# Optimization experiments

Hardware: AMD Instinct MI355X
Metric: run time of the kernel (lower is better)

## Reference

```python
import jax, jax.numpy as jnp
import numpy as np

N_NODES = 100000
N_FEAT = 256
N_HIDDEN = 64
N_EDGES = 3200000
LEAKY_SLOPE = 0.05


def setup_inputs() -> dict:
    key = jax.random.key(0)
    k1, k2, k3, k4, k5 = jax.random.split(key, 5)
    x = jax.random.normal(k1, (N_NODES, N_FEAT), dtype=jnp.float32)
    edge_index = jax.random.randint(k2, (2, N_EDGES), 0, N_NODES, dtype=jnp.int64)
    # params (torch Linear default-like scale)
    W_fc = jax.random.normal(k3, (N_FEAT, N_HIDDEN), dtype=jnp.float32) / np.sqrt(N_FEAT)
    a_w = jax.random.normal(k4, (2 * N_HIDDEN, 1), dtype=jnp.float32) / np.sqrt(2 * N_HIDDEN)
    a_b = jax.random.normal(k5, (1,), dtype=jnp.float32) * 0.01
    return {"x": x, "edge_index": edge_index, "W_fc": W_fc, "a_w": a_w, "a_b": a_b}


def reference(x, edge_index, W_fc, a_w, a_b):
    n = x.shape[0]
    h = x @ W_fc                                  # [N, H]
    src = edge_index[0]
    dst = edge_index[1]
    # a([h_src, h_dst]) == h_src @ a_w[:H] + h_dst @ a_w[H:] + a_b (same math, avoids concat)
    s = h @ a_w[:N_HIDDEN, 0]                     # [N]
    t = h @ a_w[N_HIDDEN:, 0]                     # [N]
    e = s[src] + t[dst] + a_b[0]                  # [E]
    e = jnp.where(e >= 0, e, LEAKY_SLOPE * e)     # LeakyReLU(0.05)
    attention = jnp.exp(e)                        # [E]
    row_sum = jax.ops.segment_sum(attention, src, num_segments=n)  # [N]
    alpha = attention / row_sum[src]              # [E]
    # sparse mm: out[i] = sum_{e: src_e=i} alpha_e * h[dst_e]
    out = jax.ops.segment_sum(alpha[:, None] * h[dst], src, num_segments=n)  # [N, H]
    return out, alpha
```

## Files before the change

kernel.cpp:

```cpp
#include <hip/hip_runtime.h>
#include <hip/hip_fp16.h>
#include <cstdint>
#include <cstddef>

#define NFEAT 256
#define NHID 64
#define SLOPE 0.05f
#define BKTSZ 64
#define NBKT_MAX 1568
#define P1 512
#define DSTBITS 17
#define WTPAD 264
#define SORTBUF 6272
#define BKTCAP 2560

typedef _Float16 half8 __attribute__((ext_vector_type(8)));
typedef float f32x4 __attribute__((ext_vector_type(4)));

__global__ __launch_bounds__(256) void fc_kernel(
    const float* __restrict__ x, const float* __restrict__ W,
    const float* __restrict__ aw,
    __half* __restrict__ h, float* __restrict__ srinv, float* __restrict__ t,
    int nNodes)
{
    __shared__ _Float16 Wt[NHID][WTPAD];

    const int tid = threadIdx.x;

    #pragma unroll 4
    for (int it = 0; it < 16; ++it) {
        const int idx = it * 256 + tid;
        const int n  = idx & 63;
        const int k0 = (idx >> 6) << 2;
        union { _Float16 v[4]; uint2 u; } pk;
        pk.v[0] = (_Float16)W[(k0 + 0) * NHID + n];
        pk.v[1] = (_Float16)W[(k0 + 1) * NHID + n];
        pk.v[2] = (_Float16)W[(k0 + 2) * NHID + n];
        pk.v[3] = (_Float16)W[(k0 + 3) * NHID + n];
        *(uint2*)&Wt[n][k0] = pk.u;
    }
    __syncthreads();

    const int l   = tid & 63;
    const int wv  = tid >> 6;
    const int l16 = l & 15;
    const int q   = l >> 4;
    const int kb8 = q * 8;

    const int blockRow = blockIdx.x * 128;
    const int nClamp = nNodes - 1;
    const int r0c = min(blockRow + wv * 32 + l16,      nClamp);
    const int r1c = min(blockRow + wv * 32 + l16 + 16, nClamp);
    const float* xr0 = x + (size_t)r0c * NFEAT;
    const float* xr1 = x + (size_t)r1c * NFEAT;

    f32x4 acc[2][4];
    #pragma unroll
    for (int m = 0; m < 2; ++m)
        #pragma unroll
        for (int nb = 0; nb < 4; ++nb)
            acc[m][nb] = (f32x4){0.f, 0.f, 0.f, 0.f};

    #pragma unroll
    for (int ks = 0; ks < 8; ++ks) {
        const int k0 = ks * 32 + kb8;
        const float4 fa0 = *(const float4*)(xr0 + k0);
        const float4 fa1 = *(const float4*)(xr0 + k0 + 4);
        const float4 fb0 = *(const float4*)(xr1 + k0);
        const float4 fb1 = *(const float4*)(xr1 + k0 + 4);
        half8 a0, a1;
        a0[0] = (_Float16)fa0.x; a0[1] = (_Float16)fa0.y;
        a0[2] = (_Float16)fa0.z; a0[3] = (_Float16)fa0.w;
        a0[4] = (_Float16)fa1.x; a0[5] = (_Float16)fa1.y;
        a0[6] = (_Float16)fa1.z; a0[7] = (_Float16)fa1.w;
        a1[0] = (_Float16)fb0.x; a1[1] = (_Float16)fb0.y;
        a1[2] = (_Float16)fb0.z; a1[3] = (_Float16)fb0.w;
        a1[4] = (_Float16)fb1.x; a1[5] = (_Float16)fb1.y;
        a1[6] = (_Float16)fb1.z; a1[7] = (_Float16)fb1.w;
        const half8 b0 = *(const half8*)&Wt[ 0 + l16][k0];
        const half8 b1 = *(const half8*)&Wt[16 + l16][k0];
        const half8 b2 = *(const half8*)&Wt[32 + l16][k0];
        const half8 b3 = *(const half8*)&Wt[48 + l16][k0];
        acc[0][0] = __builtin_amdgcn_mfma_f32_16x16x32_f16(a0, b0, acc[0][0], 0, 0, 0);
        acc[0][1] = __builtin_amdgcn_mfma_f32_16x16x32_f16(a0, b1, acc[0][1], 0, 0, 0);
        acc[0][2] = __builtin_amdgcn_mfma_f32_16x16x32_f16(a0, b2, acc[0][2], 0, 0, 0);
        acc[0][3] = __builtin_amdgcn_mfma_f32_16x16x32_f16(a0, b3, acc[0][3], 0, 0, 0);
        acc[1][0] = __builtin_amdgcn_mfma_f32_16x16x32_f16(a1, b0, acc[1][0], 0, 0, 0);
        acc[1][1] = __builtin_amdgcn_mfma_f32_16x16x32_f16(a1, b1, acc[1][1], 0, 0, 0);
        acc[1][2] = __builtin_amdgcn_mfma_f32_16x16x32_f16(a1, b2, acc[1][2], 0, 0, 0);
        acc[1][3] = __builtin_amdgcn_mfma_f32_16x16x32_f16(a1, b3, acc[1][3], 0, 0, 0);
    }

    const float aws0 = aw[l16],      aws1 = aw[16 + l16];
    const float aws2 = aw[32 + l16], aws3 = aw[48 + l16];
    const float awt0 = aw[64 + l16], awt1 = aw[80 + l16];
    const float awt2 = aw[96 + l16], awt3 = aw[112 + l16];

    #pragma unroll
    for (int m = 0; m < 2; ++m) {
        const int rb = blockRow + wv * 32 + m * 16 + q * 4;
        #pragma unroll
        for (int r = 0; r < 4; ++r) {
            const int row = rb + r;
            const bool ok = row < nNodes;
            const float c0 = acc[m][0][r];
            const float c1 = acc[m][1][r];
            const float c2 = acc[m][2][r];
            const float c3 = acc[m][3][r];
            if (ok) {
                __half* hp = &h[(size_t)row * NHID + l16];
                hp[0]  = __float2half(c0);
                hp[16] = __float2half(c1);
                hp[32] = __float2half(c2);
                hp[48] = __float2half(c3);
            }
            float ps = c0 * aws0 + c1 * aws1 + c2 * aws2 + c3 * aws3;
            float pt = c0 * awt0 + c1 * awt1 + c2 * awt2 + c3 * awt3;
            ps += __shfl_xor(ps, 1, 16); pt += __shfl_xor(pt, 1, 16);
            ps += __shfl_xor(ps, 2, 16); pt += __shfl_xor(pt, 2, 16);
            ps += __shfl_xor(ps, 4, 16); pt += __shfl_xor(pt, 4, 16);
            ps += __shfl_xor(ps, 8, 16); pt += __shfl_xor(pt, 8, 16);
            if (ok && l16 == 0) { srinv[2 * row] = ps; t[row] = pt; }
        }
    }
}

__global__ __launch_bounds__(256) void cnt_kernel(
    const int* __restrict__ ei, int E, int CPB, int nbkt, int* __restrict__ cntT)
{
    __shared__ int hist[NBKT_MAX];
    const int g = blockIdx.x;
    const int tid = threadIdx.x;
    for (int i = tid; i < nbkt; i += 256) hist[i] = 0;
    __syncthreads();
    const int beg = g * CPB;
    const int end = min(E, beg + CPB);
    const int c4 = (end - beg) >> 2;
    for (int i = tid; i < c4; i += 256) {
        const int4 v = *(const int4*)&ei[beg + i * 4];
        atomicAdd(&hist[v.x >> 6], 1);
        atomicAdd(&hist[v.y >> 6], 1);
        atomicAdd(&hist[v.z >> 6], 1);
        atomicAdd(&hist[v.w >> 6], 1);
    }
    for (int e = beg + c4 * 4 + tid; e < end; e += 256)
        atomicAdd(&hist[ei[e] >> 6], 1);
    __syncthreads();
    for (int b = tid; b < nbkt; b += 256)
        cntT[b * P1 + g] = hist[b];
}

__global__ __launch_bounds__(256) void scanA_kernel(
    const int* __restrict__ v, int* __restrict__ bsum, int n)
{
    __shared__ int sh[256];
    const int i = blockIdx.x * 256 + threadIdx.x;
    sh[threadIdx.x] = (i < n) ? v[i] : 0;
    __syncthreads();
    #pragma unroll
    for (int off = 128; off > 0; off >>= 1) {
        if (threadIdx.x < off) sh[threadIdx.x] += sh[threadIdx.x + off];
        __syncthreads();
    }
    if (threadIdx.x == 0) bsum[blockIdx.x] = sh[0];
}

__global__ __launch_bounds__(256) void scanC_kernel(
    const int* __restrict__ v, const int* __restrict__ bsum,
    int* __restrict__ outp, int n, int NB)
{
    __shared__ int red[256];
    __shared__ int sh[256];
    __shared__ int base0s;
    const int tid = threadIdx.x;

    int partial = 0;
    for (int j = tid; j < (int)blockIdx.x; j += 256) partial += bsum[j];
    red[tid] = partial;
    __syncthreads();
    #pragma unroll
    for (int off = 128; off > 0; off >>= 1) {
        if (tid < off) red[tid] += red[tid + off];
        __syncthreads();
    }
    if (tid == 0) base0s = red[0];
    __syncthreads();
    const int base0 = base0s;

    const int i = blockIdx.x * 256 + tid;
    const int val = (i < n) ? v[i] : 0;
    sh[tid] = val;
    __syncthreads();
    #pragma unroll
    for (int off = 1; off < 256; off <<= 1) {
        int add = (tid >= off) ? sh[tid - off] : 0;
        __syncthreads();
        sh[tid] += add;
        __syncthreads();
    }
    const int incl = sh[tid];
    if (i < n) outp[i] = base0 + incl - val;
    if (i == n - 1) outp[n] = base0 + incl;
}

__global__ __launch_bounds__(256) void place_kernel(
    const int* __restrict__ ei, int E, int CPB, int nbkt,
    const int* __restrict__ cntT, const int* __restrict__ base,
    int* __restrict__ pairs)
{
    __shared__ int loff[NBKT_MAX + 1];
    __shared__ int cur[NBKT_MAX];
    __shared__ int gb[NBKT_MAX];
    __shared__ int psum[256];
    __shared__ int sorted[SORTBUF];

    const int g = blockIdx.x;
    const int tid = threadIdx.x;
    const int beg = g * CPB;
    const int end = min(E, beg + CPB);
    const int total = end - beg;
    const int CHK = (nbkt + 255) / 256;

    for (int b = tid; b < nbkt; b += 256) {
        loff[b] = cntT[b * P1 + g];
        gb[b]   = base[b * P1 + g];
    }
    __syncthreads();

    {
        int mysum = 0;
        const int b0 = tid * CHK;
        const int b1 = min(b0 + CHK, nbkt);
        for (int b = b0; b < b1; ++b) mysum += loff[b];
        psum[tid] = mysum;
        __syncthreads();
        #pragma unroll
        for (int o = 1; o < 256; o <<= 1) {
            int v = 0;
            if (tid >= o) v = psum[tid - o];
            __syncthreads();
            psum[tid] += v;
            __syncthreads();
        }
        int run = (tid > 0) ? psum[tid - 1] : 0;
        for (int b = b0; b < b1; ++b) {
            const int c = loff[b];
            loff[b] = run;
            cur[b] = run;
            run += c;
        }
        if (tid == 255) loff[nbkt] = run;
    }
    __syncthreads();

    const int c4 = total >> 2;
    for (int i = tid; i < c4; i += 256) {
        const int e = beg + i * 4;
        const int4 s4 = *(const int4*)&ei[e];
        const int4 d4 = *(const int4*)&ei[E + e];
        int p;
        p = atomicAdd(&cur[s4.x >> 6], 1); sorted[p] = ((s4.x & (BKTSZ-1)) << DSTBITS) | d4.x;
        p = atomicAdd(&cur[s4.y >> 6], 1); sorted[p] = ((s4.y & (BKTSZ-1)) << DSTBITS) | d4.y;
        p = atomicAdd(&cur[s4.z >> 6], 1); sorted[p] = ((s4.z & (BKTSZ-1)) << DSTBITS) | d4.z;
        p = atomicAdd(&cur[s4.w >> 6], 1); sorted[p] = ((s4.w & (BKTSZ-1)) << DSTBITS) | d4.w;
    }
    for (int e = beg + c4 * 4 + tid; e < end; e += 256) {
        const int sn = ei[e];
        const int d  = ei[E + e];
        const int p  = atomicAdd(&cur[sn >> 6], 1);
        sorted[p] = ((sn & (BKTSZ-1)) << DSTBITS) | d;
    }
    __syncthreads();

    for (int i = tid; i < total; i += 256) {
        int lo = 0, hi = nbkt;
        #pragma unroll
        for (int it = 0; it < 11; ++it) {
            const int mid = (lo + hi) >> 1;
            if (loff[mid] <= i) lo = mid; else hi = mid;
        }
        pairs[gb[lo] + (i - loff[lo])] = sorted[i];
    }
}

__global__ __launch_bounds__(256) void bagg_kernel(
    const int* __restrict__ pairs, const int* __restrict__ base,
    float* __restrict__ srinv, const float* __restrict__ t,
    const __half* __restrict__ h, const float* __restrict__ ab_p,
    float* __restrict__ out, int nNodes, int nbkt, int E)
{
    __shared__ int cnt[BKTSZ];
    __shared__ int off[BKTSZ];
    __shared__ int cur[BKTSZ];
    __shared__ int sorted[BKTCAP];

    const int bkt = blockIdx.x;
    const int tid = threadIdx.x;
    const int beg = base[bkt * P1];
    const int end = (bkt + 1 < nbkt) ? base[(bkt + 1) * P1] : E;

    if (tid < BKTSZ) cnt[tid] = 0;
    __syncthreads();

    int pr[10];
    int myc = 0;
    #pragma unroll
    for (int k = 0; k < 10; ++k) {
        const int e = beg + k * 256 + tid;
        if (e < end) {
            const int p = pairs[e];
            pr[k] = p;
            atomicAdd(&cnt[p >> DSTBITS], 1);
            myc = k + 1;
        }
    }
    __syncthreads();

    if (tid < BKTSZ) off[tid] = cnt[tid];
    __syncthreads();
    #pragma unroll
    for (int o = 1; o < BKTSZ; o <<= 1) {
        int v = 0;
        if (tid < BKTSZ && tid >= o) v = off[tid - o];
        __syncthreads();
        if (tid < BKTSZ) off[tid] += v;
        __syncthreads();
    }
    if (tid < BKTSZ) cur[tid] = off[tid] - cnt[tid];
    __syncthreads();

    #pragma unroll
    for (int k = 0; k < 10; ++k) {
        if (k < myc) {
            const int p = pr[k];
            const int pos = atomicAdd(&cur[p >> DSTBITS], 1);
            sorted[pos] = p & ((1 << DSTBITS) - 1);
        }
    }
    __syncthreads();

    const int lane = tid & 63;
    const int wv = tid >> 6;
    const int quarter = lane >> 4;
    const int col = lane & 15;
    const float ab = ab_p[0];
    const uint2* hh4 = (const uint2*)h;

    for (int li = wv; li < BKTSZ; li += 4) {
        const int n = (bkt << 6) + li;
        if (n >= nNodes) continue;
        const int endL = off[li];
        const int begL = endL - cnt[li];
        const float sn = srinv[2 * n];
        float part = 0.f;
        float4 acc = {0.f, 0.f, 0.f, 0.f};
        for (int i0 = begL; i0 < endL; i0 += 64) {
            const int my = min(endL - i0, 64);
            int dl = 0; float el = 0.f;
            if (lane < my) {
                dl = sorted[i0 + lane];
                float ev = sn + t[dl] + ab;
                ev = (ev >= 0.f) ? ev : SLOPE * ev;
                el = __expf(ev);
            }
            part += el;
            const int my4 = (my + 3) & ~3;
            int j = 0;
            for (; j + 8 <= my4; j += 8) {
                const int   d0 = __shfl(dl, j + quarter);
                const float e0 = __shfl(el, j + quarter);
                const int   d1 = __shfl(dl, j + 4 + quarter);
                const float e1 = __shfl(el, j + 4 + quarter);
                const uint2 r0 = hh4[(size_t)d0 * 16 + col];
                const uint2 r1 = hh4[(size_t)d1 * 16 + col];
                const float2 lo0 = __half22float2(*(const __half2*)&r0.x);
                const float2 hi0 = __half22float2(*(const __half2*)&r0.y);
                const float2 lo1 = __half22float2(*(const __half2*)&r1.x);
                const float2 hi1 = __half22float2(*(const __half2*)&r1.y);
                acc.x += e0 * lo0.x; acc.y += e0 * lo0.y;
                acc.z += e0 * hi0.x; acc.w += e0 * hi0.y;
                acc.x += e1 * lo1.x; acc.y += e1 * lo1.y;
                acc.z += e1 * hi1.x; acc.w += e1 * hi1.y;
            }
            for (; j < my4; j += 4) {
                const int   d0 = __shfl(dl, j + quarter);
                const float e0 = __shfl(el, j + quarter);
                const uint2 r0 = hh4[(size_t)d0 * 16 + col];
                const float2 lo0 = __half22float2(*(const __half2*)&r0.x);
                const float2 hi0 = __half22float2(*(const __half2*)&r0.y);
                acc.x += e0 * lo0.x; acc.y += e0 * lo0.y;
                acc.z += e0 * hi0.x; acc.w += e0 * hi0.y;
            }
        }
        #pragma unroll
        for (int o = 32; o > 0; o >>= 1) part += __shfl_xor(part, o, 64);
        const float inv = (endL > begL) ? 1.0f / part : 0.f;
        if (lane == 0) srinv[2 * n + 1] = inv;
        acc.x += __shfl_xor(acc.x, 16, 64); acc.x += __shfl_xor(acc.x, 32, 64);
        acc.y += __shfl_xor(acc.y, 16, 64); acc.y += __shfl_xor(acc.y, 32, 64);
        acc.z += __shfl_xor(acc.z, 16, 64); acc.z += __shfl_xor(acc.z, 32, 64);
        acc.w += __shfl_xor(acc.w, 16, 64); acc.w += __shfl_xor(acc.w, 32, 64);
        if (quarter == 0) {
            float4 o4;
            o4.x = acc.x * inv; o4.y = acc.y * inv;
            o4.z = acc.z * inv; o4.w = acc.w * inv;
            *(float4*)&out[(size_t)n * NHID + col * 4] = o4;
        }
    }
}

__global__ __launch_bounds__(256) void alpha_kernel(
    const int* __restrict__ ei, const float* __restrict__ srinv,
    const float* __restrict__ t,
    const float* __restrict__ ab_p, float* __restrict__ alpha, int E)
{
    const float ab = ab_p[0];
    const int gid = blockIdx.x * blockDim.x + threadIdx.x;
    const int step = gridDim.x * blockDim.x;
    const int E4 = E >> 2;

    #define AEDGE(sn, d) ({                                                 \
        const float2 sr = *(const float2*)&srinv[2 * (sn)];                 \
        float ev = sr.x + t[d] + ab;                                        \
        ev = (ev >= 0.f) ? ev : SLOPE * ev;                                 \
        __expf(ev) * sr.y; })

    for (int i = gid; i < E4; i += step) {
        const int e = i * 4;
        const int4 s4 = *(const int4*)&ei[e];
        const int4 d4 = *(const int4*)&ei[E + e];
        float4 a;
        a.x = AEDGE(s4.x, d4.x);
        a.y = AEDGE(s4.y, d4.y);
        a.z = AEDGE(s4.z, d4.z);
        a.w = AEDGE(s4.w, d4.w);
        *(float4*)&alpha[e] = a;
    }
    for (int e = E4 * 4 + gid; e < E; e += step) {
        const int sn = ei[e];
        const int d = ei[E + e];
        alpha[e] = AEDGE(sn, d);
    }
}

extern "C" void kernel_launch(void* const* d_in, const int* in_sizes, int n_in,
                              void* d_out, int out_size, void* d_ws, size_t ws_size,
                              hipStream_t stream)
{
    const float* x  = (const float*)d_in[0];
    const int*   ei = (const int*)d_in[1];
    const float* W  = (const float*)d_in[2];
    const float* aw = (const float*)d_in[3];
    const float* ab = (const float*)d_in[4];

    const int nNodes = in_sizes[0] / NFEAT;
    const int E      = in_sizes[1] / 2;
    const int NBfc   = (nNodes + 127) / 128;
    const int nbkt   = (nNodes + BKTSZ - 1) / BKTSZ;
    const int CPB    = ((E + P1 - 1) / P1 + 3) & ~3;
    const int nScan  = nbkt * P1;
    const int NBs    = (nScan + 255) / 256;

    float* out   = (float*)d_out;
    float* alpha = out + (size_t)nNodes * NHID;

    __half* h      = (__half*)d_ws;
    float* srinv   = (float*)(h + (size_t)nNodes * NHID);
    float* t       = srinv + 2 * nNodes;
    int*   cntT    = (int*)(t + nNodes);
    int*   base    = cntT + nScan;
    int*   bsum    = base + nScan + 4;
    int*   pairs   = bsum + NBs;

    fc_kernel<<<NBfc, 256, 0, stream>>>(x, W, aw, h, srinv, t, nNodes);
    cnt_kernel<<<P1, 256, 0, stream>>>(ei, E, CPB, nbkt, cntT);
    scanA_kernel<<<NBs, 256, 0, stream>>>(cntT, bsum, nScan);
    scanC_kernel<<<NBs, 256, 0, stream>>>(cntT, bsum, base, nScan, NBs);
    place_kernel<<<P1, 256, 0, stream>>>(ei, E, CPB, nbkt, cntT, base, pairs);
    bagg_kernel<<<nbkt, 256, 0, stream>>>(pairs, base, srinv, t, h, ab,
                                          out, nNodes, nbkt, E);
    alpha_kernel<<<2048, 256, 0, stream>>>(ei, srinv, t, ab, alpha, E);
}
```

Baseline: 176.0 us.

## Precompute edge exponentials into LDS and halve partition block count

```diff
diff --git a/kernel.cpp b/kernel.cpp
--- a/kernel.cpp
+++ b/kernel.cpp
@@ -8,10 +8,11 @@
 #define SLOPE 0.05f
 #define BKTSZ 64
 #define NBKT_MAX 1568
-#define P1 512
+#define P1 256
 #define DSTBITS 17
+#define DSTMASK ((1 << DSTBITS) - 1)
 #define WTPAD 264
-#define SORTBUF 6272
+#define SORTBUF 12504
 #define BKTCAP 2560
 
 typedef _Float16 half8 __attribute__((ext_vector_type(8)));
@@ -289,17 +290,24 @@
     const __half* __restrict__ h, const float* __restrict__ ab_p,
     float* __restrict__ out, int nNodes, int nbkt, int E)
 {
-    __shared__ int cnt[BKTSZ];
-    __shared__ int off[BKTSZ];
-    __shared__ int cur[BKTSZ];
-    __shared__ int sorted[BKTCAP];
+    __shared__ int   cnt[BKTSZ];
+    __shared__ int   off[BKTSZ];
+    __shared__ int   cur[BKTSZ];
+    __shared__ float s_l[BKTSZ];
+    __shared__ int   sorted[BKTCAP];
+    __shared__ float elds[BKTCAP];
 
     const int bkt = blockIdx.x;
     const int tid = threadIdx.x;
     const int beg = base[bkt * P1];
     const int end = (bkt + 1 < nbkt) ? base[(bkt + 1) * P1] : E;
-
-    if (tid < BKTSZ) cnt[tid] = 0;
+    const int total = end - beg;
+
+    if (tid < BKTSZ) {
+        cnt[tid] = 0;
+        const int n = (bkt << 6) + tid;
+        s_l[tid] = (n < nNodes) ? srinv[2 * n] : 0.f;
+    }
     __syncthreads();
 
     int pr[10];
@@ -334,8 +342,17 @@
         if (k < myc) {
             const int p = pr[k];
             const int pos = atomicAdd(&cur[p >> DSTBITS], 1);
-            sorted[pos] = p & ((1 << DSTBITS) - 1);
-        }
+            sorted[pos] = p;
+        }
+    }
+    __syncthreads();
+
+    const float ab = ab_p[0];
+    for (int i = tid; i < total; i += 256) {
+        const int p = sorted[i];
+        float ev = s_l[p >> DSTBITS] + t[p & DSTMASK] + ab;
+        ev = (ev >= 0.f) ? ev : SLOPE * ev;
+        elds[i] = __expf(ev);
     }
     __syncthreads();
 
@@ -343,7 +360,6 @@
     const int wv = tid >> 6;
     const int quarter = lane >> 4;
     const int col = lane & 15;
-    const float ab = ab_p[0];
     const uint2* hh4 = (const uint2*)h;
 
     for (int li = wv; li < BKTSZ; li += 4) {
@@ -351,50 +367,37 @@
         if (n >= nNodes) continue;
         const int endL = off[li];
         const int begL = endL - cnt[li];
-        const float sn = srinv[2 * n];
         float part = 0.f;
         float4 acc = {0.f, 0.f, 0.f, 0.f};
-        for (int i0 = begL; i0 < endL; i0 += 64) {
-            const int my = min(endL - i0, 64);
-            int dl = 0; float el = 0.f;
-            if (lane < my) {
-                dl = sorted[i0 + lane];
-                float ev = sn + t[dl] + ab;
-                ev = (ev >= 0.f) ? ev : SLOPE * ev;
-                el = __expf(ev);
+        int i0 = begL;
+        for (; i0 + 16 <= endL; i0 += 16) {
+            #pragma unroll
+            for (int u = 0; u < 4; ++u) {
+                const int idx = i0 + u * 4 + quarter;
+                const int p = sorted[idx];
+                const float el = elds[idx];
+                const uint2 r = hh4[(size_t)(p & DSTMASK) * 16 + col];
+                const float2 lo = __half22float2(*(const __half2*)&r.x);
+                const float2 hi = __half22float2(*(const __half2*)&r.y);
+                part += el;
+                acc.x += el * lo.x; acc.y += el * lo.y;
+                acc.z += el * hi.x; acc.w += el * hi.y;
             }
+        }
+        for (; i0 < endL; i0 += 4) {
+            const int idx = i0 + quarter;
+            int p = 0; float el = 0.f;
+            if (idx < endL) { p = sorted[idx]; el = elds[idx]; }
+            const uint2 r = hh4[(size_t)(p & DSTMASK) * 16 + col];
+            const float2 lo = __half22float2(*(const __half2*)&r.x);
+            const float2 hi = __half22float2(*(const __half2*)&r.y);
             part += el;
-            const int my4 = (my + 3) & ~3;
-            int j = 0;
-            for (; j + 8 <= my4; j += 8) {
-                const int   d0 = __shfl(dl, j + quarter);
-                const float e0 = __shfl(el, j + quarter);
-                const int   d1 = __shfl(dl, j + 4 + quarter);
-                const float e1 = __shfl(el, j + 4 + quarter);
-                const uint2 r0 = hh4[(size_t)d0 * 16 + col];
-                const uint2 r1 = hh4[(size_t)d1 * 16 + col];
-                const float2 lo0 = __half22float2(*(const __half2*)&r0.x);
-                const float2 hi0 = __half22float2(*(const __half2*)&r0.y);
-                const float2 lo1 = __half22float2(*(const __half2*)&r1.x);
-                const float2 hi1 = __half22float2(*(const __half2*)&r1.y);
-                acc.x += e0 * lo0.x; acc.y += e0 * lo0.y;
-                acc.z += e0 * hi0.x; acc.w += e0 * hi0.y;
-                acc.x += e1 * lo1.x; acc.y += e1 * lo1.y;
-                acc.z += e1 * hi1.x; acc.w += e1 * hi1.y;
-            }
-            for (; j < my4; j += 4) {
-                const int   d0 = __shfl(dl, j + quarter);
-                const float e0 = __shfl(el, j + quarter);
-                const uint2 r0 = hh4[(size_t)d0 * 16 + col];
-                const float2 lo0 = __half22float2(*(const __half2*)&r0.x);
-                const float2 hi0 = __half22float2(*(const __half2*)&r0.y);
-                acc.x += e0 * lo0.x; acc.y += e0 * lo0.y;
-                acc.z += e0 * hi0.x; acc.w += e0 * hi0.y;
-            }
+            acc.x += el * lo.x; acc.y += el * lo.y;
+            acc.z += el * hi.x; acc.w += el * hi.y;
         }
         #pragma unroll
         for (int o = 32; o > 0; o >>= 1) part += __shfl_xor(part, o, 64);
-        const float inv = (endL > begL) ? 1.0f / part : 0.f;
+        const float inv = (endL > begL) ? 16.0f / part : 0.f;
         if (lane == 0) srinv[2 * n + 1] = inv;
         acc.x += __shfl_xor(acc.x, 16, 64); acc.x += __shfl_xor(acc.x, 32, 64);
         acc.y += __shfl_xor(acc.y, 16, 64); acc.y += __shfl_xor(acc.y, 32, 64);
```

Result: no change. 178.5 us (+1.4%).
